# Kernel tuning notes

Hardware: AMD Instinct MI355X
Metric: run time of the kernel (lower is better)

## Reference

```python
import jax, jax.numpy as jnp
import numpy as np

B, C, H, W = 2, 64, 64, 128
HW = H * W
PCR = (0.0, -25.6, -3.0, 51.2, 25.6, 1.0)  # point cloud range x/y/z min, x/y/z max
VOX = (0.1, 0.1, 4.0)                      # voxel size
NX = int(round((PCR[3] - PCR[0]) / VOX[0]))  # 512
NY = int(round((PCR[4] - PCR[1]) / VOX[1]))  # 512
BIG = 1e10  # masked-out distance (avoid inf for clean vjp)


def _rand_points(key):
    k_xyz, k_i = jax.random.split(key)
    u = jax.random.uniform(k_xyz, (B, 3, H, W), jnp.float32)
    lo = jnp.array([PCR[0], PCR[1], PCR[2]], jnp.float32).reshape(1, 3, 1, 1)
    hi = jnp.array([PCR[3], PCR[4], PCR[5]], jnp.float32).reshape(1, 3, 1, 1)
    xyz = lo + u * (hi - lo)
    inten = jax.random.uniform(k_i, (B, 1, H, W), jnp.float32)
    return jnp.concatenate([xyz, inten], axis=1)  # (B,4,H,W)


def setup_inputs() -> dict:
    key = jax.random.key(0)
    k1, k2, k3, k4, k5 = jax.random.split(key, 5)
    return {
        "fv_features": jax.random.normal(k1, (B, C, H, W), jnp.float32),
        "points_img": _rand_points(k2),
        "proj_masks": jax.random.randint(k4, (B, H, W), 0, 2).astype(jnp.int32),
        "points_img_far": _rand_points(k3),
        "proj_masks_far": jax.random.randint(k5, (B, H, W), 0, 2).astype(jnp.int32),
    }


def _three_interpolate(near_pts, near_feats, near_valid, far_pts):
    """pointnet2 three_nn + three_interpolate with invalid near points masked.
    near_pts: (N,3), near_feats: (N,C), near_valid: (N,) bool, far_pts: (M,3).
    Returns interpolated far features (M,C)."""
    # squared distances via |a|^2 + |b|^2 - 2 a.b  -> (M, N), avoids (M,N,3) temp
    d2 = (jnp.sum(far_pts * far_pts, -1)[:, None]
          + jnp.sum(near_pts * near_pts, -1)[None, :]
          - 2.0 * far_pts @ near_pts.T)
    d2 = jnp.where(near_valid[None, :], d2, BIG)
    neg_d, idx = jax.lax.top_k(-d2, 3)        # 3 nearest near-points per far point
    dist = -neg_d                              # squared dists, as in pointnet2 CUDA
    dist_recip = 1.0 / (dist + 1e-8)
    weight = dist_recip / jnp.sum(dist_recip, axis=-1, keepdims=True)  # (M,3)
    gathered = near_feats[idx]                 # (M,3,C)
    return jnp.einsum('mk,mkc->mc', weight, gathered)


def _scatter_bev(pts, feats, valid):
    """Mean-scatter point features into the BEV grid. pts:(N,3) feats:(N,C) valid:(N,)."""
    ix = jnp.floor((pts[:, 0] - PCR[0]) / VOX[0]).astype(jnp.int32)
    iy = jnp.floor((pts[:, 1] - PCR[1]) / VOX[1]).astype(jnp.int32)
    in_range = (ix >= 0) & (ix < NX) & (iy >= 0) & (iy < NY)
    w = (valid & in_range).astype(feats.dtype)            # zero-weight invalid pts
    flat = jnp.clip(iy, 0, NY - 1) * NX + jnp.clip(ix, 0, NX - 1)
    sums = jnp.zeros((NY * NX, feats.shape[1]), feats.dtype).at[flat].add(feats * w[:, None])
    cnt = jnp.zeros((NY * NX,), feats.dtype).at[flat].add(w)
    bev = sums / jnp.maximum(cnt, 1.0)[:, None]
    return bev.reshape(NY, NX, -1).transpose(2, 0, 1)      # (C, NY, NX)


def reference(fv_features, points_img, proj_masks, points_img_far, proj_masks_far):
    feats = fv_features.transpose(0, 2, 3, 1).reshape(B, HW, C)
    pts = points_img[:, :3].transpose(0, 2, 3, 1).reshape(B, HW, 3)
    pts_far = points_img_far[:, :3].transpose(0, 2, 3, 1).reshape(B, HW, 3)
    m = proj_masks.reshape(B, HW) > 0
    m_far = proj_masks_far.reshape(B, HW) > 0
    outs = []
    for k in range(B):  # small fixed batch loop, mirrors original per-sample loop
        interp = _three_interpolate(pts[k], feats[k], m[k], pts_far[k])
        all_pts = jnp.concatenate([pts[k], pts_far[k]], axis=0)
        all_feats = jnp.concatenate([feats[k], interp], axis=0)
        all_valid = jnp.concatenate([m[k], m_far[k]], axis=0)
        outs.append(_scatter_bev(all_pts, all_feats, all_valid))
    return jnp.stack(outs, axis=0)  # (B, C, NY, NX)
```

## Files before the change

### kernel.cpp

```cpp
#include <hip/hip_runtime.h>
#include <math.h>

constexpr int B_  = 2;
constexpr int C_  = 64;
constexpr int HW_ = 64 * 128;
constexpr int N_  = HW_;
constexpr int NX_ = 512;
constexpr int NY_ = 512;
constexpr int NYNX_ = NX_ * NY_;
constexpr int GC_  = 32;
constexpr int GCC_ = GC_ * GC_;
constexpr int LPF_ = 8;

__device__ __forceinline__ int voxel_of(float x, float y, float w) {
#pragma clang fp contract(off)
  if (w == 0.0f) return -1;
  float qx = (x - 0.0f) / 0.1f;
  float qy = (y - (-25.6f)) / 0.1f;
  int ix = (int)floorf(qx);
  int iy = (int)floorf(qy);
  if (ix < 0 || ix >= NX_ || iy < 0 || iy >= NY_) return -1;
  return iy * NX_ + ix;
}

__device__ __forceinline__ int gcell_x(float x) {
  int c = (int)floorf(x * 0.625f);
  return min(GC_ - 1, max(0, c));
}
__device__ __forceinline__ int gcell_y(float y) {
  int c = (int)floorf((y + 25.6f) * 0.625f);
  return min(GC_ - 1, max(0, c));
}

__global__ __launch_bounds__(256) void prep_kernel(
    const float* __restrict__ fv,
    const float* __restrict__ pi, const int* __restrict__ pm,
    const float* __restrict__ pif, const int* __restrict__ pmf,
    float4* __restrict__ near4, float4* __restrict__ far4,
    float4* __restrict__ nearnn, float* __restrict__ cnt,
    float* __restrict__ fvT) {
#pragma clang fp contract(off)
  __shared__ float tile[64][65];
  if (blockIdx.x < 64) {
    int t = blockIdx.x * 256 + threadIdx.x;
    int k = t / N_, n = t % N_;
    const float* base  = pi  + (size_t)k * 4 * HW_;
    const float* basef = pif + (size_t)k * 4 * HW_;
    float x = base[n], y = base[HW_ + n], z = base[2 * HW_ + n];
    bool v = pm[k * HW_ + n] > 0;
    near4[t] = make_float4(x, y, z, v ? 1.0f : 0.0f);
    float sq = (x * x + y * y) + z * z;
    nearnn[t] = v ? make_float4(x, y, z, sq)
                 : make_float4(0.0f, 0.0f, 0.0f, 1e10f);
    float fx = basef[n], fy = basef[HW_ + n], fz = basef[2 * HW_ + n];
    bool vf = pmf[k * HW_ + n] > 0;
    far4[t] = make_float4(fx, fy, fz, vf ? 1.0f : 0.0f);

    int vn = voxel_of(x, y, v ? 1.0f : 0.0f);
    if (vn >= 0) atomicAdd(&cnt[(size_t)k * NYNX_ + vn], 1.0f);
    int vfv = voxel_of(fx, fy, vf ? 1.0f : 0.0f);
    if (vfv >= 0) atomicAdd(&cnt[(size_t)k * NYNX_ + vfv], 1.0f);
  } else {
    int bid = blockIdx.x - 64;
    int k = bid >> 7;
    int n0 = (bid & 127) * 64;
    int tx = threadIdx.x & 63, ty = threadIdx.x >> 6;
    for (int c = ty; c < C_; c += 4)
      tile[c][tx] = fv[((size_t)(k * C_ + c)) * HW_ + n0 + tx];
    __syncthreads();
    for (int nn = ty; nn < 64; nn += 4)
      fvT[((size_t)(k * HW_ + n0 + nn)) * C_ + tx] = tile[tx][nn];
  }
}

__device__ __forceinline__ void merge3L(float tv, int idx,
                                        float& b0, float& b1, float& b2,
                                        int& i0, int& i1, int& i2) {
  bool w0 = (tv < b0) || (tv == b0 && idx < i0);
  bool w1 = (tv < b1) || (tv == b1 && idx < i1);
  bool w2 = (tv < b2) || (tv == b2 && idx < i2);
  float ob0 = b0, ob1 = b1;
  int   oi0 = i0, oi1 = i1;
  b0 = w0 ? tv : b0;                    i0 = w0 ? idx : i0;
  b1 = w0 ? ob0 : (w1 ? tv : b1);       i1 = w0 ? oi0 : (w1 ? idx : i1);
  b2 = w1 ? ob1 : (w2 ? tv : b2);       i2 = w1 ? oi1 : (w2 ? idx : i2);
}

__global__ __launch_bounds__(256) void build_grid_kernel(
    const float4* __restrict__ nearnn, const float* __restrict__ cnt,
    int* __restrict__ cell_start, float4* __restrict__ gpts,
    int* __restrict__ gidx, float* __restrict__ acc) {
  __shared__ int lcnt[GCC_];
  __shared__ int lsum[256];
  __shared__ int lcur[GCC_];
  int t = threadIdx.x;
  if (blockIdx.x < (unsigned)B_) {
    int k = blockIdx.x;
    for (int i = t; i < GCC_; i += 256) lcnt[i] = 0;
    __syncthreads();
    for (int n = t; n < N_; n += 256) {
      float4 q = nearnn[k * N_ + n];
      if (q.w < 1e9f)
        atomicAdd(&lcnt[gcell_y(q.y) * GC_ + gcell_x(q.x)], 1);
    }
    __syncthreads();
    int base = t * 4;
    int c0 = lcnt[base], c1 = lcnt[base + 1], c2 = lcnt[base + 2], c3 = lcnt[base + 3];
    int s = c0 + c1 + c2 + c3;
    lsum[t] = s;
    __syncthreads();
    for (int off = 1; off < 256; off <<= 1) {
      int v = (t >= off) ? lsum[t - off] : 0;
      __syncthreads();
      lsum[t] += v;
      __syncthreads();
    }
    int ex = lsum[t] - s;
    lcnt[base] = ex;
    lcnt[base + 1] = ex + c0;
    lcnt[base + 2] = ex + c0 + c1;
    lcnt[base + 3] = ex + c0 + c1 + c2;
    __syncthreads();
    for (int i = t; i < GCC_; i += 256) {
      cell_start[k * (GCC_ + 1) + i] = lcnt[i];
      lcur[i] = lcnt[i];
    }
    if (t == 255) cell_start[k * (GCC_ + 1) + GCC_] = lsum[255];
    __syncthreads();
    for (int n = t; n < N_; n += 256) {
      float4 q = nearnn[k * N_ + n];
      if (q.w < 1e9f) {
        int c = gcell_y(q.y) * GC_ + gcell_x(q.x);
        int p = atomicAdd(&lcur[c], 1);
        gpts[k * N_ + p] = q;
        gidx[k * N_ + p] = n;
      }
    }
  } else {
    int tt = (blockIdx.x - B_) * 256 + t;
    if (cnt[tt] >= 2.0f) {
      float4* row = (float4*)(acc + (size_t)tt * C_);
      float4 z = make_float4(0.0f, 0.0f, 0.0f, 0.0f);
      for (int i = 0; i < C_ / 4; ++i) row[i] = z;
    }
  }
}

__global__ __launch_bounds__(256) void nn_search_kernel(
    const float4* __restrict__ far4, const int* __restrict__ cell_start,
    const float4* __restrict__ gpts, const int* __restrict__ gidx,
    int* __restrict__ nn_idx, float* __restrict__ nn_w) {
#pragma clang fp contract(off)
  int tid = threadIdx.x;
  int q = tid & (LPF_ - 1);
  int g = blockIdx.x * (256 / LPF_) + (tid / LPF_);
  int k = g >> 13;
  int m = g & (N_ - 1);

  float4 f = far4[k * N_ + m];
  float sf = (f.x * f.x + f.y * f.y) + f.z * f.z;
  float ax = 2.0f * f.x, ay = 2.0f * f.y, az = 2.0f * f.z;
  int fcx = gcell_x(f.x), fcy = gcell_y(f.y);
  const int* cs_ = cell_start + k * (GCC_ + 1);

  float b0 = 1e30f, b1 = 1e30f, b2 = 1e30f;
  int i0 = 0, i1 = 0, i2 = 0;

  for (int r = 0; r < GC_; ++r) {
    int nc = (r == 0) ? 1 : 8 * r;
    for (int i = q; i < nc; i += LPF_) {
      int dx, dy;
      if (r == 0)            { dx = 0;             dy = 0; }
      else if (i < 2*r + 1)  { dx = i - r;         dy = -r; }
      else if (i < 4*r + 2)  { dx = i - (3*r + 1); dy = r; }
      else if (i < 6*r + 1)  { dx = -r;            dy = i - (5*r + 1); }
      else                   { dx = r;             dy = i - 7*r; }
      int cx = fcx + dx, cy = fcy + dy;
      if (cx < 0 || cx >= GC_ || cy < 0 || cy >= GC_) continue;
      int c = cy * GC_ + cx;
      int s = cs_[c], e = cs_[c + 1];
      for (int j = s; j < e; ++j) {
        float4 p = gpts[k * N_ + j];
        int idx = gidx[k * N_ + j];
        float p0 = ax * p.x;
        float mm = __builtin_fmaf(az, p.z, __builtin_fmaf(ay, p.y, p0));
        float tv = (sf + p.w) - mm;
        merge3L(tv, idx, b0, b1, b2, i0, i1, i2);
      }
    }
    float s2 = b2;
    s2 = fminf(s2, __shfl_xor(s2, 1));
    s2 = fminf(s2, __shfl_xor(s2, 2));
    s2 = fminf(s2, __shfl_xor(s2, 4));
    float rd = (float)r * 1.6f;
    if (rd * rd > s2 + 0.01f) break;
  }

  int base = tid & ~(LPF_ - 1);
  for (int s = 1; s < LPF_; ++s) {
    float v0 = __shfl(b0, base + s), v1 = __shfl(b1, base + s), v2 = __shfl(b2, base + s);
    int   j0 = __shfl(i0, base + s), j1 = __shfl(i1, base + s), j2 = __shfl(i2, base + s);
    if (q == 0) {
      merge3L(v0, j0, b0, b1, b2, i0, i1, i2);
      merge3L(v1, j1, b0, b1, b2, i0, i1, i2);
      merge3L(v2, j2, b0, b1, b2, i0, i1, i2);
    }
  }
  if (q == 0) {
    float r0 = 1.0f / (b0 + 1e-8f);
    float r1 = 1.0f / (b1 + 1e-8f);
    float r2 = 1.0f / (b2 + 1e-8f);
    float rs = (r0 + r1) + r2;
    int o = g * 3;
    nn_idx[o] = i0; nn_idx[o + 1] = i1; nn_idx[o + 2] = i2;
    nn_w[o] = r0 / rs; nn_w[o + 1] = r1 / rs; nn_w[o + 2] = r2 / rs;
  }
}

__global__ __launch_bounds__(256) void scatter_feat_kernel(
    const float4* __restrict__ near4, const float4* __restrict__ far4,
    const float* __restrict__ fvT,
    const int* __restrict__ nn_idx, const float* __restrict__ nn_w,
    const float* __restrict__ cnt, float* __restrict__ acc) {
#pragma clang fp contract(off)
  int lane = threadIdx.x & 63;
  int wv = blockIdx.x * 4 + (threadIdx.x >> 6);
  int k = wv / (2 * N_);
  int p = wv % (2 * N_);
  bool is_far = p >= N_;
  int n = is_far ? p - N_ : p;

  float4 pt = is_far ? far4[k * N_ + n] : near4[k * N_ + n];
  int v = voxel_of(pt.x, pt.y, pt.w);
  if (v < 0) return;

  float val;
  if (!is_far) {
    val = fvT[((size_t)(k * N_ + n)) * C_ + lane];
  } else {
    int o = (k * N_ + n) * 3;
    int i0 = nn_idx[o], i1 = nn_idx[o + 1], i2 = nn_idx[o + 2];
    float w0 = nn_w[o], w1 = nn_w[o + 1], w2 = nn_w[o + 2];
    val = w0 * fvT[((size_t)(k * N_ + i0)) * C_ + lane]
        + w1 * fvT[((size_t)(k * N_ + i1)) * C_ + lane]
        + w2 * fvT[((size_t)(k * N_ + i2)) * C_ + lane];
  }
  size_t rowoff = ((size_t)k * NYNX_ + v) * C_;
  float cn = cnt[(size_t)k * NYNX_ + v];
  if (cn == 1.0f) acc[rowoff + lane] = val;
  else            atomicAdd(&acc[rowoff + lane], val);
}

__global__ __launch_bounds__(256) void emit_kernel(
    const float* __restrict__ acc, const float* __restrict__ cnt,
    float* __restrict__ out) {
#pragma clang fp contract(off)
  __shared__ float tile[64][65];
  __shared__ float cs[64];
  int t = threadIdx.x;
  int k = blockIdx.y;
  int v0 = blockIdx.x * 64;

  if (t < 64) cs[t] = cnt[(size_t)k * NYNX_ + v0 + t];
  __syncthreads();

  const float4* acc4 = (const float4*)acc;
#pragma unroll
  for (int p = 0; p < 4; ++p) {
    int row = p * 16 + (t >> 4);
    int f4  = t & 15;
    float c = cs[row];
    float4 a = make_float4(0.0f, 0.0f, 0.0f, 0.0f);
    if (c > 0.0f) {
      a = acc4[((size_t)k * NYNX_ + v0 + row) * (C_ / 4) + f4];
      a.x /= c; a.y /= c; a.z /= c; a.w /= c;
    }
    tile[f4 * 4 + 0][row] = a.x;
    tile[f4 * 4 + 1][row] = a.y;
    tile[f4 * 4 + 2][row] = a.z;
    tile[f4 * 4 + 3][row] = a.w;
  }
  __syncthreads();

#pragma unroll
  for (int p = 0; p < 4; ++p) {
    int c  = p * 16 + (t >> 4);
    int xq = t & 15;
    float4 o = make_float4(tile[c][xq * 4 + 0], tile[c][xq * 4 + 1],
                           tile[c][xq * 4 + 2], tile[c][xq * 4 + 3]);
    ((float4*)out)[(((size_t)k * C_ + c) * NYNX_ + v0) / 4 + xq] = o;
  }
}

extern "C" void kernel_launch(void* const* d_in, const int* in_sizes, int n_in,
                              void* d_out, int out_size, void* d_ws, size_t ws_size,
                              hipStream_t stream) {
  const float* fv  = (const float*)d_in[0];
  const float* pi  = (const float*)d_in[1];
  const int*   pm  = (const int*)d_in[2];
  const float* pif = (const float*)d_in[3];
  const int*   pmf = (const int*)d_in[4];
  float* out = (float*)d_out;

  char* wsb = (char*)d_ws;
  float*  fvT    = (float*)(wsb);
  float*  cnt    = (float*)(wsb + 4194304);
  float4* near4  = (float4*)(wsb + 6291456);
  float4* far4   = (float4*)(wsb + 6553600);
  float4* nearnn = (float4*)(wsb + 6815744);
  int*    nnidx  = (int*)(wsb + 7077888);
  float*  nnw    = (float*)(wsb + 7274496);
  int*    cstart = (int*)(wsb + 7471104);
  int*    gidx   = (int*)(wsb + 7479424);
  float4* gpts   = (float4*)(wsb + 7544960);
  float*  acc    = (float*)(wsb + 8388608);

  hipMemsetAsync(cnt, 0, (size_t)B_ * NYNX_ * sizeof(float), stream);

  prep_kernel<<<320, 256, 0, stream>>>(
      fv, pi, pm, pif, pmf, near4, far4, nearnn, cnt, fvT);
  build_grid_kernel<<<B_ + B_ * NYNX_ / 256, 256, 0, stream>>>(
      nearnn, cnt, cstart, gpts, gidx, acc);
  nn_search_kernel<<<B_ * N_ * LPF_ / 256, 256, 0, stream>>>(
      far4, cstart, gpts, gidx, nnidx, nnw);
  scatter_feat_kernel<<<B_ * 2 * N_ / 4, 256, 0, stream>>>(
      near4, far4, fvT, nnidx, nnw, cnt, acc);
  emit_kernel<<<dim3(NYNX_ / 64, B_), 256, 0, stream>>>(acc, cnt, out);
}
```

Baseline: 211.3 us.

## Fuse nearest-neighbor search with far-point feature scatter into one kernel

Merges the three-NN search and the scatter of interpolated far features into a single kernel. Each 8-lane group now broadcasts its weights and indices, then scatters its own 64-channel row as float4 chunks. Near-point scatter runs in extra blocks of the same launch. This removes one launch and the nn_idx/nn_w round trip through global memory. In exchange, far-point scatter uses only 8 lanes per point with 4 scalar atomics each, and it sits in the same grid as the longer-running search blocks.

```diff
diff --git a/kernel.cpp b/kernel.cpp
--- a/kernel.cpp
+++ b/kernel.cpp
@@ -11,6 +11,8 @@
 constexpr int GC_  = 32;
 constexpr int GCC_ = GC_ * GC_;
 constexpr int LPF_ = 8;
+constexpr int BN_  = B_ * N_;
+constexpr int NNB_ = BN_ / (256 / LPF_);
 
 __device__ __forceinline__ int voxel_of(float x, float y, float w) {
 #pragma clang fp contract(off)
@@ -146,109 +148,117 @@
   }
 }
 
-__global__ __launch_bounds__(256) void nn_search_kernel(
+__global__ __launch_bounds__(256) void nn_scatter_kernel(
     const float4* __restrict__ far4, const int* __restrict__ cell_start,
     const float4* __restrict__ gpts, const int* __restrict__ gidx,
-    int* __restrict__ nn_idx, float* __restrict__ nn_w) {
+    const float4* __restrict__ near4, const float* __restrict__ fvT,
+    const float* __restrict__ cnt, float* __restrict__ acc) {
 #pragma clang fp contract(off)
   int tid = threadIdx.x;
-  int q = tid & (LPF_ - 1);
-  int g = blockIdx.x * (256 / LPF_) + (tid / LPF_);
-  int k = g >> 13;
-  int m = g & (N_ - 1);
-
-  float4 f = far4[k * N_ + m];
-  float sf = (f.x * f.x + f.y * f.y) + f.z * f.z;
-  float ax = 2.0f * f.x, ay = 2.0f * f.y, az = 2.0f * f.z;
-  int fcx = gcell_x(f.x), fcy = gcell_y(f.y);
-  const int* cs_ = cell_start + k * (GCC_ + 1);
-
-  float b0 = 1e30f, b1 = 1e30f, b2 = 1e30f;
-  int i0 = 0, i1 = 0, i2 = 0;
-
-  for (int r = 0; r < GC_; ++r) {
-    int nc = (r == 0) ? 1 : 8 * r;
-    for (int i = q; i < nc; i += LPF_) {
-      int dx, dy;
-      if (r == 0)            { dx = 0;             dy = 0; }
-      else if (i < 2*r + 1)  { dx = i - r;         dy = -r; }
-      else if (i < 4*r + 2)  { dx = i - (3*r + 1); dy = r; }
-      else if (i < 6*r + 1)  { dx = -r;            dy = i - (5*r + 1); }
-      else                   { dx = r;             dy = i - 7*r; }
-      int cx = fcx + dx, cy = fcy + dy;
-      if (cx < 0 || cx >= GC_ || cy < 0 || cy >= GC_) continue;
-      int c = cy * GC_ + cx;
-      int s = cs_[c], e = cs_[c + 1];
-      for (int j = s; j < e; ++j) {
-        float4 p = gpts[k * N_ + j];
-        int idx = gidx[k * N_ + j];
-        float p0 = ax * p.x;
-        float mm = __builtin_fmaf(az, p.z, __builtin_fmaf(ay, p.y, p0));
-        float tv = (sf + p.w) - mm;
-        merge3L(tv, idx, b0, b1, b2, i0, i1, i2);
+  if (blockIdx.x < (unsigned)NNB_) {
+    int q = tid & (LPF_ - 1);
+    int g = blockIdx.x * (256 / LPF_) + (tid / LPF_);
+    int k = g >> 13;
+    int m = g & (N_ - 1);
+
+    float4 f = far4[k * N_ + m];
+    float sf = (f.x * f.x + f.y * f.y) + f.z * f.z;
+    float ax = 2.0f * f.x, ay = 2.0f * f.y, az = 2.0f * f.z;
+    int fcx = gcell_x(f.x), fcy = gcell_y(f.y);
+    const int* cs_ = cell_start + k * (GCC_ + 1);
+
+    float b0 = 1e30f, b1 = 1e30f, b2 = 1e30f;
+    int i0 = 0, i1 = 0, i2 = 0;
+
+    for (int r = 0; r < GC_; ++r) {
+      int nc = (r == 0) ? 1 : 8 * r;
+      for (int i = q; i < nc; i += LPF_) {
+        int dx, dy;
+        if (r == 0)            { dx = 0;             dy = 0; }
+        else if (i < 2*r + 1)  { dx = i - r;         dy = -r; }
+        else if (i < 4*r + 2)  { dx = i - (3*r + 1); dy = r; }
+        else if (i < 6*r + 1)  { dx = -r;            dy = i - (5*r + 1); }
+        else                   { dx = r;             dy = i - 7*r; }
+        int cx = fcx + dx, cy = fcy + dy;
+        if (cx < 0 || cx >= GC_ || cy < 0 || cy >= GC_) continue;
+        int c = cy * GC_ + cx;
+        int s = cs_[c], e = cs_[c + 1];
+        for (int j = s; j < e; ++j) {
+          float4 p = gpts[k * N_ + j];
+          int idx = gidx[k * N_ + j];
+          float p0 = ax * p.x;
+          float mm = __builtin_fmaf(az, p.z, __builtin_fmaf(ay, p.y, p0));
+          float tv = (sf + p.w) - mm;
+          merge3L(tv, idx, b0, b1, b2, i0, i1, i2);
+        }
       }
-    }
-    float s2 = b2;
-    s2 = fminf(s2, __shfl_xor(s2, 1));
-    s2 = fminf(s2, __shfl_xor(s2, 2));
-    s2 = fminf(s2, __shfl_xor(s2, 4));
-    float rd = (float)r * 1.6f;
-    if (rd * rd > s2 + 0.01f) break;
-  }
-
-  int base = tid & ~(LPF_ - 1);
-  for (int s = 1; s < LPF_; ++s) {
-    float v0 = __shfl(b0, base + s), v1 = __shfl(b1, base + s), v2 = __shfl(b2, base + s);
-    int   j0 = __shfl(i0, base + s), j1 = __shfl(i1, base + s), j2 = __shfl(i2, base + s);
+      float s2 = b2;
+      s2 = fminf(s2, __shfl_xor(s2, 1));
+      s2 = fminf(s2, __shfl_xor(s2, 2));
+      s2 = fminf(s2, __shfl_xor(s2, 4));
+      float rd = (float)r * 1.6f;
+      if (rd * rd > s2 + 0.01f) break;
+    }
+
+    int base = tid & ~(LPF_ - 1);
+    for (int s = 1; s < LPF_; ++s) {
+      float v0 = __shfl(b0, base + s), v1 = __shfl(b1, base + s), v2 = __shfl(b2, base + s);
+      int   j0 = __shfl(i0, base + s), j1 = __shfl(i1, base + s), j2 = __shfl(i2, base + s);
+      if (q == 0) {
+        merge3L(v0, j0, b0, b1, b2, i0, i1, i2);
+        merge3L(v1, j1, b0, b1, b2, i0, i1, i2);
+        merge3L(v2, j2, b0, b1, b2, i0, i1, i2);
+      }
+    }
+    float w0_ = 0.0f, w1_ = 0.0f, w2_ = 0.0f;
     if (q == 0) {
-      merge3L(v0, j0, b0, b1, b2, i0, i1, i2);
-      merge3L(v1, j1, b0, b1, b2, i0, i1, i2);
-      merge3L(v2, j2, b0, b1, b2, i0, i1, i2);
-    }
-  }
-  if (q == 0) {
-    float r0 = 1.0f / (b0 + 1e-8f);
-    float r1 = 1.0f / (b1 + 1e-8f);
-    float r2 = 1.0f / (b2 + 1e-8f);
-    float rs = (r0 + r1) + r2;
-    int o = g * 3;
-    nn_idx[o] = i0; nn_idx[o + 1] = i1; nn_idx[o + 2] = i2;
-    nn_w[o] = r0 / rs; nn_w[o + 1] = r1 / rs; nn_w[o + 2] = r2 / rs;
-  }
-}
-
-__global__ __launch_bounds__(256) void scatter_feat_kernel(
-    const float4* __restrict__ near4, const float4* __restrict__ far4,
-    const float* __restrict__ fvT,
-    const int* __restrict__ nn_idx, const float* __restrict__ nn_w,
-    const float* __restrict__ cnt, float* __restrict__ acc) {
-#pragma clang fp contract(off)
-  int lane = threadIdx.x & 63;
-  int wv = blockIdx.x * 4 + (threadIdx.x >> 6);
-  int k = wv / (2 * N_);
-  int p = wv % (2 * N_);
-  bool is_far = p >= N_;
-  int n = is_far ? p - N_ : p;
-
-  float4 pt = is_far ? far4[k * N_ + n] : near4[k * N_ + n];
-  int v = voxel_of(pt.x, pt.y, pt.w);
-  if (v < 0) return;
-
-  float val;
-  if (!is_far) {
-    val = fvT[((size_t)(k * N_ + n)) * C_ + lane];
+      float r0 = 1.0f / (b0 + 1e-8f);
+      float r1 = 1.0f / (b1 + 1e-8f);
+      float r2 = 1.0f / (b2 + 1e-8f);
+      float rs = (r0 + r1) + r2;
+      w0_ = r0 / rs; w1_ = r1 / rs; w2_ = r2 / rs;
+    }
+    float w0 = __shfl(w0_, base), w1 = __shfl(w1_, base), w2 = __shfl(w2_, base);
+    int   j0 = __shfl(i0, base),  j1 = __shfl(i1, base),  j2 = __shfl(i2, base);
+
+    int v = voxel_of(f.x, f.y, f.w);
+    if (v < 0) return;
+    float cn = cnt[(size_t)k * NYNX_ + v];
+    const float4* r0p = (const float4*)(fvT + ((size_t)(k * N_ + j0)) * C_);
+    const float4* r1p = (const float4*)(fvT + ((size_t)(k * N_ + j1)) * C_);
+    const float4* r2p = (const float4*)(fvT + ((size_t)(k * N_ + j2)) * C_);
+    size_t rowoff = ((size_t)k * NYNX_ + v) * C_;
+#pragma unroll
+    for (int h = 0; h < 2; ++h) {
+      int c4 = q * 2 + h;
+      float4 a = r0p[c4], b = r1p[c4], c = r2p[c4];
+      float4 val;
+      val.x = (w0 * a.x + w1 * b.x) + w2 * c.x;
+      val.y = (w0 * a.y + w1 * b.y) + w2 * c.y;
+      val.z = (w0 * a.z + w1 * b.z) + w2 * c.z;
+      val.w = (w0 * a.w + w1 * b.w) + w2 * c.w;
+      if (cn == 1.0f) {
+        ((float4*)(acc + rowoff))[c4] = val;
+      } else {
+        float* p = acc + rowoff + c4 * 4;
+        atomicAdd(p + 0, val.x); atomicAdd(p + 1, val.y);
+        atomicAdd(p + 2, val.z); atomicAdd(p + 3, val.w);
+      }
+    }
   } else {
-    int o = (k * N_ + n) * 3;
-    int i0 = nn_idx[o], i1 = nn_idx[o + 1], i2 = nn_idx[o + 2];
-    float w0 = nn_w[o], w1 = nn_w[o + 1], w2 = nn_w[o + 2];
-    val = w0 * fvT[((size_t)(k * N_ + i0)) * C_ + lane]
-        + w1 * fvT[((size_t)(k * N_ + i1)) * C_ + lane]
-        + w2 * fvT[((size_t)(k * N_ + i2)) * C_ + lane];
-  }
-  size_t rowoff = ((size_t)k * NYNX_ + v) * C_;
-  float cn = cnt[(size_t)k * NYNX_ + v];
-  if (cn == 1.0f) acc[rowoff + lane] = val;
-  else            atomicAdd(&acc[rowoff + lane], val);
+    int lane = tid & 63;
+    int wv = (blockIdx.x - NNB_) * 4 + (tid >> 6);
+    int k = wv >> 13;
+    int n = wv & (N_ - 1);
+    float4 pt = near4[k * N_ + n];
+    int v = voxel_of(pt.x, pt.y, pt.w);
+    if (v < 0) return;
+    float val = fvT[((size_t)(k * N_ + n)) * C_ + lane];
+    size_t rowoff = ((size_t)k * NYNX_ + v) * C_;
+    float cn = cnt[(size_t)k * NYNX_ + v];
+    if (cn == 1.0f) acc[rowoff + lane] = val;
+    else            atomicAdd(&acc[rowoff + lane], val);
+  }
 }
 
 __global__ __launch_bounds__(256) void emit_kernel(
@@ -308,8 +318,6 @@
   float4* near4  = (float4*)(wsb + 6291456);
   float4* far4   = (float4*)(wsb + 6553600);
   float4* nearnn = (float4*)(wsb + 6815744);
-  int*    nnidx  = (int*)(wsb + 7077888);
-  float*  nnw    = (float*)(wsb + 7274496);
   int*    cstart = (int*)(wsb + 7471104);
   int*    gidx   = (int*)(wsb + 7479424);
   float4* gpts   = (float4*)(wsb + 7544960);
@@ -321,9 +329,7 @@
       fv, pi, pm, pif, pmf, near4, far4, nearnn, cnt, fvT);
   build_grid_kernel<<<B_ + B_ * NYNX_ / 256, 256, 0, stream>>>(
       nearnn, cnt, cstart, gpts, gidx, acc);
-  nn_search_kernel<<<B_ * N_ * LPF_ / 256, 256, 0, stream>>>(
-      far4, cstart, gpts, gidx, nnidx, nnw);
-  scatter_feat_kernel<<<B_ * 2 * N_ / 4, 256, 0, stream>>>(
-      near4, far4, fvT, nnidx, nnw, cnt, acc);
+  nn_scatter_kernel<<<NNB_ + B_ * N_ / 4, 256, 0, stream>>>(
+      far4, cstart, gpts, gidx, near4, fvT, cnt, acc);
   emit_kernel<<<dim3(NYNX_ / 64, B_), 256, 0, stream>>>(acc, cnt, out);
 }
```

Result: faster. 204.3 us (-3.3%).
